# Kernel tuning notes

Measured on AMD Instinct MI355X. Metric: run time of the kernel, lower is better.

Reference implementation:

```python
import jax, jax.numpy as jnp
import numpy as np

EPS_LN = 1e-5  # nn.LayerNorm default eps
EPS_AD = 1e-5  # AdaIN calc_mean_std eps


def calc_mean_std(feat):
    # feat: [B, S, D]; instance-norm style stats per channel over the seq axis
    mean = jnp.mean(feat, axis=1, keepdims=True)
    var = jnp.var(feat, axis=1, keepdims=True, ddof=1)  # torch .var() is unbiased
    return mean, jnp.sqrt(var + EPS_AD)


def adain(content, style):
    c_mean, c_std = calc_mean_std(content)
    s_mean, s_std = calc_mean_std(style)
    return (content - c_mean) / c_std * s_std + s_mean


def layernorm(x, g, b):
    mu = jnp.mean(x, axis=-1, keepdims=True)
    var = jnp.mean(jnp.square(x - mu), axis=-1, keepdims=True)
    return (x - mu) * jax.lax.rsqrt(var + EPS_LN) * g + b


def silu(x):
    return x * jax.nn.sigmoid(x)


def setup_inputs() -> dict:
    B, S, D = 64, 256, 1024
    key = jax.random.key(0)
    ks = jax.random.split(key, 8)
    sc = lambda n: 1.0 / np.sqrt(n)
    return {
        "x": jax.random.normal(ks[0], (B, S, 2 * D), jnp.float32),
        "embed": jax.random.normal(ks[1], (B, S, D), jnp.float32),
        "style_code": jax.random.normal(ks[2], (B, S, D), jnp.float32),
        # conct: Linear(2*dim, dim)
        "Wc": jax.random.normal(ks[3], (D, 2 * D), jnp.float32) * sc(2 * D),
        "bc": jnp.zeros((D,), jnp.float32),
        # emb_fc: Linear(dim, dim)
        "We": jax.random.normal(ks[4], (D, D), jnp.float32) * sc(D),
        "be": jnp.zeros((D,), jnp.float32),
        # fc0: Conv1d(seq0, seq1, 1) -> [seq1, seq0] matrix over the seq axis
        "W0": jax.random.normal(ks[5], (S, S), jnp.float32) * sc(S),
        "b0": jnp.zeros((S,), jnp.float32),
        # fc1: Linear(dim, dim)
        "W1": jax.random.normal(ks[6], (D, D), jnp.float32) * sc(D),
        "b1": jnp.zeros((D,), jnp.float32),
        # LayerNorm affine params
        "g0": jnp.ones((D,), jnp.float32),
        "beta0": jnp.zeros((D,), jnp.float32),
        "g1": jnp.ones((D,), jnp.float32),
        "beta1": jnp.zeros((D,), jnp.float32),
    }


def reference(x, embed, style_code, Wc, bc, We, be, W0, b0, W1, b1, g0, beta0, g1, beta1):
    # conct (first=True): [B,S,2D] -> [B,S,D]
    adain_input = jnp.einsum('bse,de->bsd', x, Wc) + bc
    tmp = adain(adain_input, style_code)  # alpha = 1.0 so tmp replaces adain_input
    x = tmp + (jnp.einsum('bsd,ed->bse', silu(embed), We) + be)
    # block 0: LN -> 1x1 Conv1d over seq axis -> SiLU -> residual
    x_ = layernorm(x, g0, beta0)
    x_ = jnp.einsum('ts,bsd->btd', W0, x_) + b0[:, None]
    x = x + silu(x_)
    # block 1: LN -> Linear over dim axis -> SiLU -> residual
    x_ = layernorm(x, g1, beta1)
    x_ = jnp.einsum('bsd,ed->bse', x_, W1) + b1
    x = x + silu(x_)
    return (x, embed, style_code)
```

## Files before the change

### kernel.cpp

```cpp
#include <hip/hip_runtime.h>
#include <cstddef>
#include <cstdint>

#define BB 64
#define SS 256
#define DD 1024
#define MM (BB * SS)

typedef unsigned short u16;
typedef unsigned int u32;
typedef short bf16x8 __attribute__((ext_vector_type(8)));
typedef float f32x4 __attribute__((ext_vector_type(4)));

__device__ __forceinline__ float silu_f(float v) {
    return v * (1.0f / (1.0f + __expf(-v)));
}

__device__ __forceinline__ int swz4(int r) {
    return ((r >> 2) & 3) ^ (r & 3);
}

__device__ __forceinline__ void splitf(float f, u16& h, u16& l) {
    const u32 b = __float_as_uint(f);
    const u32 hb = b & 0xFFFF0000u;
    const float lf = f - __uint_as_float(hb);
    h = (u16)(hb >> 16);
    l = (u16)(__float_as_uint(lf) >> 16);
}

__device__ __forceinline__ void gll16(const void* g, void* l) {
    __builtin_amdgcn_global_load_lds(
        (const __attribute__((address_space(1))) u32*)g,
        (__attribute__((address_space(3))) u32*)l, 16, 0, 0);
}

__device__ __forceinline__ void cvt16(const float* av, uint4& h0, uint4& h1,
                                      uint4& l0, uint4& l1) {
    u16 hh[16], hl[16];
#pragma unroll
    for (int m = 0; m < 16; ++m) splitf(av[m], hh[m], hl[m]);
    u32 ph[8], pl[8];
#pragma unroll
    for (int m = 0; m < 8; ++m) {
        ph[m] = (u32)hh[2 * m] | ((u32)hh[2 * m + 1] << 16);
        pl[m] = (u32)hl[2 * m] | ((u32)hl[2 * m + 1] << 16);
    }
    h0 = make_uint4(ph[0], ph[1], ph[2], ph[3]);
    h1 = make_uint4(ph[4], ph[5], ph[6], ph[7]);
    l0 = make_uint4(pl[0], pl[1], pl[2], pl[3]);
    l1 = make_uint4(pl[4], pl[5], pl[6], pl[7]);
}

__global__ __launch_bounds__(256)
void split_w(const float* __restrict__ src, u16* __restrict__ dh,
             u16* __restrict__ dl, int k8shift)
{
    const int idx = blockIdx.x * 256 + threadIdx.x;
    const int n = idx >> k8shift;
    const int c = idx & ((1 << k8shift) - 1);
    const int srcc = (c & ~3) | ((c & 3) ^ swz4(n & 15));
    const float* sp = src + ((size_t)n << (k8shift + 3)) + srcc * 8;
    const float4 v0 = *(const float4*)sp;
    const float4 v1 = *(const float4*)(sp + 4);
    const float av[8] = {v0.x, v0.y, v0.z, v0.w, v1.x, v1.y, v1.z, v1.w};
    u16 hh[8], hl[8];
#pragma unroll
    for (int m = 0; m < 8; ++m) splitf(av[m], hh[m], hl[m]);
    u32 ph[4], pl[4];
#pragma unroll
    for (int m = 0; m < 4; ++m) {
        ph[m] = (u32)hh[2 * m] | ((u32)hh[2 * m + 1] << 16);
        pl[m] = (u32)hl[2 * m] | ((u32)hl[2 * m + 1] << 16);
    }
    *(uint4*)&dh[(size_t)idx * 8] = make_uint4(ph[0], ph[1], ph[2], ph[3]);
    *(uint4*)&dl[(size_t)idx * 8] = make_uint4(pl[0], pl[1], pl[2], pl[3]);
}

template<int AM, int BM, int EPI>
__global__ __launch_bounds__(256, (AM == 0 && BM == 0) ? 4 : 3)
void gemm_bf3(const float* __restrict__ A32,
              const u16* __restrict__ Ahg, const u16* __restrict__ Alg,
              const float* __restrict__ B32,
              const u16* __restrict__ Bhg, const u16* __restrict__ Blg,
              const float* __restrict__ bias,
              const float* __restrict__ t0, const float* __restrict__ scl,
              const float* __restrict__ shf,
              const float* __restrict__ resid, float* __restrict__ C,
              int M, int N, int K, long long bsB, long long bsC)
{
    __shared__ u16 lds[16384];

    const int z = blockIdx.z;
    const int nbx = gridDim.x;
    const int nwg = nbx * gridDim.y;
    int lin = blockIdx.y * nbx + blockIdx.x;
    if ((nwg & 7) == 0) {
        const int cpx = nwg >> 3;
        lin = (lin & 7) * cpx + (lin >> 3);
    }
    const int bx = lin % nbx;
    const int by = lin / nbx;
    const int row0 = by * 128, col0 = bx * 128;

    const int tid = threadIdx.x;
    const int lane = tid & 63, wid = tid >> 6;
    const int wr = wid >> 1, wc = wid & 1;
    const int fr = lane & 15, fh = lane >> 4;
    const int fsw = (fh ^ swz4(fr)) * 8;

    const int srow = tid >> 1;
    const int sko = (tid & 1) << 4;
    const int ssw = swz4(srow & 15);
    const int sw0 = srow * 32 + (((sko >> 3) + 0) ^ ssw) * 8;
    const int sw1 = srow * 32 + (((sko >> 3) + 1) ^ ssw) * 8;

    const float* Ag32 = nullptr;
    const float* Bg32 = nullptr;
    if constexpr (AM != 0) Ag32 = A32 + (size_t)(row0 + srow) * K + sko;
    if constexpr (BM != 0) Bg32 = B32 + (size_t)(col0 + srow) * K + sko;

    const u16* gPre = nullptr; int ldsPre = 0;
    const u16* gB = nullptr; int ldsB = 0, sib0 = 0;

    if constexpr (AM == 0) {
        if constexpr (BM == 0) {
            const u16* gs; int base, lb;
            if (wid == 0)      { gs = Ahg; base = row0; lb = 0; }
            else if (wid == 1) { gs = Alg; base = row0; lb = 4096; }
            else if (wid == 2) { gs = Bhg + (size_t)z * (size_t)bsB; base = col0; lb = 8192; }
            else               { gs = Blg + (size_t)z * (size_t)bsB; base = col0; lb = 12288; }
            gPre = gs + (size_t)(base + (lane >> 2)) * K + (lane & 3) * 8;
            ldsPre = lb;
        } else {
            const u16* gs = (wid & 1) ? Alg : Ahg;
            gPre = gs + (size_t)(row0 + (lane >> 2)) * K + (lane & 3) * 8;
            ldsPre = (wid & 1) ? 4096 : 0;
        }
    } else {
        gB = ((wid < 2) ? Bhg : Blg) + (size_t)z * (size_t)bsB
             + (size_t)(col0 + (wid & 1) * 64 + (lane >> 2)) * K + (lane & 3) * 8;
        ldsB = (wid < 2) ? 8192 : 12288;
        sib0 = (wid & 1) * 4;
    }

    f32x4 acc[4][4];
#pragma unroll
    for (int i = 0; i < 4; ++i)
#pragma unroll
        for (int j = 0; j < 4; ++j) acc[i][j] = (f32x4){0.f, 0.f, 0.f, 0.f};

    for (int k0 = 0; k0 < K; k0 += 32) {
        float av[16], bv[16];
        if constexpr (AM != 0) {
            const float4 a0 = *(const float4*)(Ag32 + k0);
            const float4 a1 = *(const float4*)(Ag32 + k0 + 4);
            const float4 a2 = *(const float4*)(Ag32 + k0 + 8);
            const float4 a3 = *(const float4*)(Ag32 + k0 + 12);
            av[0]=a0.x; av[1]=a0.y; av[2]=a0.z; av[3]=a0.w;
            av[4]=a1.x; av[5]=a1.y; av[6]=a1.z; av[7]=a1.w;
            av[8]=a2.x; av[9]=a2.y; av[10]=a2.z; av[11]=a2.w;
            av[12]=a3.x; av[13]=a3.y; av[14]=a3.z; av[15]=a3.w;
            if constexpr (AM == 2) {
#pragma unroll
                for (int m = 0; m < 16; ++m) av[m] = silu_f(av[m]);
            }
        }
        if constexpr (BM != 0) {
            const float4 b0 = *(const float4*)(Bg32 + k0);
            const float4 b1 = *(const float4*)(Bg32 + k0 + 4);
            const float4 b2 = *(const float4*)(Bg32 + k0 + 8);
            const float4 b3 = *(const float4*)(Bg32 + k0 + 12);
            bv[0]=b0.x; bv[1]=b0.y; bv[2]=b0.z; bv[3]=b0.w;
            bv[4]=b1.x; bv[5]=b1.y; bv[6]=b1.z; bv[7]=b1.w;
            bv[8]=b2.x; bv[9]=b2.y; bv[10]=b2.z; bv[11]=b2.w;
            bv[12]=b3.x; bv[13]=b3.y; bv[14]=b3.z; bv[15]=b3.w;
        }

        __syncthreads();

        if constexpr (AM == 0) {
            if constexpr (BM == 0) {
#pragma unroll
                for (int q = 0; q < 8; ++q)
                    gll16(gPre + (size_t)q * 16 * K + k0, &lds[ldsPre + q * 512]);
            } else {
                if (wid < 2) {
#pragma unroll
                    for (int q = 0; q < 8; ++q)
                        gll16(gPre + (size_t)q * 16 * K + k0, &lds[ldsPre + q * 512]);
                }
            }
        } else {
#pragma unroll
            for (int q = 0; q < 4; ++q)
                gll16(gB + (size_t)q * 16 * K + k0, &lds[ldsB + (sib0 + q) * 512]);
        }

        if constexpr (AM != 0) {
            uint4 h0, h1, l0, l1;
            cvt16(av, h0, h1, l0, l1);
            *(uint4*)&lds[sw0] = h0;
            *(uint4*)&lds[sw1] = h1;
            *(uint4*)&lds[4096 + sw0] = l0;
            *(uint4*)&lds[4096 + sw1] = l1;
        }
        if constexpr (BM != 0) {
            uint4 h0, h1, l0, l1;
            cvt16(bv, h0, h1, l0, l1);
            *(uint4*)&lds[8192 + sw0] = h0;
            *(uint4*)&lds[8192 + sw1] = h1;
            *(uint4*)&lds[12288 + sw0] = l0;
            *(uint4*)&lds[12288 + sw1] = l1;
        }
        __syncthreads();

        bf16x8 fah[4], fal[4];
#pragma unroll
        for (int i = 0; i < 4; ++i) {
            const int ao = (wr * 64 + i * 16 + fr) * 32 + fsw;
            fah[i] = *(const bf16x8*)&lds[ao];
            fal[i] = *(const bf16x8*)&lds[4096 + ao];
        }
#pragma unroll
        for (int j = 0; j < 4; ++j) {
            const int bo = (wc * 64 + j * 16 + fr) * 32 + fsw;
            const bf16x8 fbh = *(const bf16x8*)&lds[8192 + bo];
            const bf16x8 fbl = *(const bf16x8*)&lds[12288 + bo];
#pragma unroll
            for (int i = 0; i < 4; ++i) {
                acc[i][j] = __builtin_amdgcn_mfma_f32_16x16x32_bf16(fah[i], fbh, acc[i][j], 0, 0, 0);
                acc[i][j] = __builtin_amdgcn_mfma_f32_16x16x32_bf16(fal[i], fbh, acc[i][j], 0, 0, 0);
                acc[i][j] = __builtin_amdgcn_mfma_f32_16x16x32_bf16(fah[i], fbl, acc[i][j], 0, 0, 0);
            }
        }
    }

    const size_t cz = (size_t)z * (size_t)bsC;
#pragma unroll
    for (int i = 0; i < 4; ++i) {
        const int rbase = row0 + wr * 64 + i * 16 + fh * 4;
#pragma unroll
        for (int j = 0; j < 4; ++j) {
            const int c = col0 + wc * 64 + j * 16 + fr;
            float bcol = 0.f, sc = 0.f, sh = 0.f;
            if constexpr (EPI != 3) bcol = bias[c];
            if constexpr (EPI == 1) {
                const int b = rbase >> 8;
                sc = scl[b * DD + c];
                sh = shf[b * DD + c];
            }
#pragma unroll
            for (int r = 0; r < 4; ++r) {
                const int rr = rbase + r;
                const size_t idx = cz + (size_t)rr * N + c;
                const float t = acc[i][j][r] + ((EPI == 3) ? bias[rr] : bcol);
                if constexpr (EPI == 0) C[idx] = t;
                else if constexpr (EPI == 1) C[idx] = fmaf(t0[idx], sc, sh) + t;
                else C[idx] = resid[idx] + silu_f(t);
            }
        }
    }
}

__global__ __launch_bounds__(256)
void adain_stats(const float* __restrict__ t0, const float* __restrict__ style,
                 float* __restrict__ scl, float* __restrict__ shf)
{
    const int idx = blockIdx.x * 256 + threadIdx.x;
    const int b = idx >> 10;
    const int d = idx & (DD - 1);
    const float* pc = t0    + (size_t)b * SS * DD + d;
    const float* ps = style + (size_t)b * SS * DD + d;
    float sc = 0.f, sc2 = 0.f, ss = 0.f, ss2 = 0.f;
    for (int s = 0; s < SS; ++s) {
        const float c  = pc[(size_t)s * DD];
        const float st = ps[(size_t)s * DD];
        sc += c;  sc2 = fmaf(c, c, sc2);
        ss += st; ss2 = fmaf(st, st, ss2);
    }
    const float mc = sc * (1.0f / SS);
    const float ms = ss * (1.0f / SS);
    float vc = (sc2 - (float)SS * mc * mc) * (1.0f / (SS - 1));
    float vs = (ss2 - (float)SS * ms * ms) * (1.0f / (SS - 1));
    vc = fmaxf(vc, 0.f);
    vs = fmaxf(vs, 0.f);
    const float csd = sqrtf(vc + 1e-5f);
    const float ssd = sqrtf(vs + 1e-5f);
    const float sca = ssd / csd;
    scl[idx] = sca;
    shf[idx] = ms - mc * sca;
}

__global__ __launch_bounds__(256)
void ln_stats(const float* __restrict__ X, float* __restrict__ mu, float* __restrict__ rs)
{
    const int row = blockIdx.x * 4 + (threadIdx.x >> 6);
    const int lane = threadIdx.x & 63;
    const float* xr = X + (size_t)row * DD;
    float sum = 0.f, sq = 0.f;
#pragma unroll
    for (int c = 0; c < 4; ++c) {
        const float4 v = *(const float4*)&xr[c * 256 + lane * 4];
        sum += v.x + v.y + v.z + v.w;
        sq += v.x * v.x + v.y * v.y + v.z * v.z + v.w * v.w;
    }
#pragma unroll
    for (int off = 32; off > 0; off >>= 1) {
        sum += __shfl_down(sum, off, 64);
        sq  += __shfl_down(sq,  off, 64);
    }
    if (lane == 0) {
        const float m = sum * (1.0f / DD);
        float var = sq * (1.0f / DD) - m * m;
        var = fmaxf(var, 0.f);
        mu[row] = m;
        rs[row] = rsqrtf(var + 1e-5f);
    }
}

__global__ __launch_bounds__(256)
void ln_t_split(const float* __restrict__ X, const float* __restrict__ mu,
                const float* __restrict__ rs, const float* __restrict__ g,
                const float* __restrict__ beta,
                u16* __restrict__ yTh, u16* __restrict__ yTl)
{
    __shared__ u16 th[64 * 66];
    __shared__ u16 tl[64 * 66];
    const int b = blockIdx.z;
    const int s0 = blockIdx.y * 64;
    const int d0 = blockIdx.x * 64;
    const int t = threadIdx.x;
    const int sl0 = t >> 4;
    const int dl4 = (t & 15) * 4;
    const float4 gv = *(const float4*)&g[d0 + dl4];
    const float4 bv = *(const float4*)&beta[d0 + dl4];
#pragma unroll
    for (int q = 0; q < 4; ++q) {
        const int s_local = q * 16 + sl0;
        const int row = b * SS + s0 + s_local;
        const float4 v = *(const float4*)&X[(size_t)row * DD + d0 + dl4];
        const float m = mu[row], r = rs[row];
        const float vals[4] = {(v.x - m) * r * gv.x + bv.x, (v.y - m) * r * gv.y + bv.y,
                               (v.z - m) * r * gv.z + bv.z, (v.w - m) * r * gv.w + bv.w};
#pragma unroll
        for (int j = 0; j < 4; ++j) {
            u16 hh, lo;
            splitf(vals[j], hh, lo);
            th[(dl4 + j) * 66 + s_local] = hh;
            tl[(dl4 + j) * 66 + s_local] = lo;
        }
    }
    __syncthreads();
    const int dl = t >> 2;
    const int sc = (t & 3) * 16;
    u32 ah[8], al[8];
#pragma unroll
    for (int jj = 0; jj < 8; ++jj) {
        ah[jj] = *(const u32*)&th[dl * 66 + sc + jj * 2];
        al[jj] = *(const u32*)&tl[dl * 66 + sc + jj * 2];
    }
    const int cc0 = (s0 + sc) >> 3;
    const int swv = swz4(dl & 15);
    const int p0 = (cc0 & ~3) | ((cc0 & 3) ^ swv);
    const int p1 = (cc0 & ~3) | ((((cc0 & 3) + 1)) ^ swv);
    const size_t rb = ((size_t)b * DD + d0 + dl) * SS;
    *(uint4*)&yTh[rb + p0 * 8] = make_uint4(ah[0], ah[1], ah[2], ah[3]);
    *(uint4*)&yTh[rb + p1 * 8] = make_uint4(ah[4], ah[5], ah[6], ah[7]);
    *(uint4*)&yTl[rb + p0 * 8] = make_uint4(al[0], al[1], al[2], al[3]);
    *(uint4*)&yTl[rb + p1 * 8] = make_uint4(al[4], al[5], al[6], al[7]);
}

__global__ __launch_bounds__(256)
void ln_split(const float* __restrict__ X, const float* __restrict__ g,
              const float* __restrict__ beta, u16* __restrict__ zh, u16* __restrict__ zl)
{
    const int row = blockIdx.x * 4 + (threadIdx.x >> 6);
    const int lane = threadIdx.x & 63;
    const float* xr = X + (size_t)row * DD;
    float4 v[4];
    float sum = 0.f, sq = 0.f;
#pragma unroll
    for (int q = 0; q < 4; ++q) {
        v[q] = *(const float4*)&xr[lane * 16 + q * 4];
        sum += v[q].x + v[q].y + v[q].z + v[q].w;
        sq += v[q].x * v[q].x + v[q].y * v[q].y + v[q].z * v[q].z + v[q].w * v[q].w;
    }
#pragma unroll
    for (int off = 32; off > 0; off >>= 1) {
        sum += __shfl_down(sum, off, 64);
        sq  += __shfl_down(sq,  off, 64);
    }
    sum = __shfl(sum, 0, 64);
    sq  = __shfl(sq,  0, 64);
    const float m = sum * (1.0f / DD);
    float var = sq * (1.0f / DD) - m * m;
    var = fmaxf(var, 0.f);
    const float r = rsqrtf(var + 1e-5f);
    float ov[16];
#pragma unroll
    for (int q = 0; q < 4; ++q) {
        const float4 gq = *(const float4*)&g[lane * 16 + q * 4];
        const float4 bq = *(const float4*)&beta[lane * 16 + q * 4];
        ov[q * 4 + 0] = (v[q].x - m) * r * gq.x + bq.x;
        ov[q * 4 + 1] = (v[q].y - m) * r * gq.y + bq.y;
        ov[q * 4 + 2] = (v[q].z - m) * r * gq.z + bq.z;
        ov[q * 4 + 3] = (v[q].w - m) * r * gq.w + bq.w;
    }
    uint4 h0, h1, l0, l1;
    cvt16(ov, h0, h1, l0, l1);
    const int swr = swz4(row & 15);
    const int c0 = lane * 2;
    const int p0 = (c0 & ~3) | ((c0 & 3) ^ swr);
    const int p1 = ((c0 + 1) & ~3) | (((c0 + 1) & 3) ^ swr);
    u16* zr = zh + (size_t)row * DD;
    u16* zr2 = zl + (size_t)row * DD;
    *(uint4*)&zr[p0 * 8]  = h0;
    *(uint4*)&zr[p1 * 8]  = h1;
    *(uint4*)&zr2[p0 * 8] = l0;
    *(uint4*)&zr2[p1 * 8] = l1;
}

__global__ __launch_bounds__(256)
void copy_pass(const float4* __restrict__ emb, const float4* __restrict__ sty,
               float4* __restrict__ out_emb, float4* __restrict__ out_sty)
{
    const int n4 = MM * DD / 4;
    const int stride = gridDim.x * blockDim.x;
    for (int i = blockIdx.x * blockDim.x + threadIdx.x; i < n4; i += stride) {
        out_emb[i] = emb[i];
        out_sty[i] = sty[i];
    }
}

extern "C" void kernel_launch(void* const* d_in, const int* in_sizes, int n_in,
                              void* d_out, int out_size, void* d_ws, size_t ws_size,
                              hipStream_t stream)
{
    const float* x     = (const float*)d_in[0];
    const float* embed = (const float*)d_in[1];
    const float* style = (const float*)d_in[2];
    const float* Wc    = (const float*)d_in[3];
    const float* bc    = (const float*)d_in[4];
    const float* We    = (const float*)d_in[5];
    const float* be    = (const float*)d_in[6];
    const float* W0    = (const float*)d_in[7];
    const float* b0    = (const float*)d_in[8];
    const float* W1    = (const float*)d_in[9];
    const float* b1    = (const float*)d_in[10];
    const float* g0    = (const float*)d_in[11];
    const float* beta0 = (const float*)d_in[12];
    const float* g1    = (const float*)d_in[13];
    const float* beta1 = (const float*)d_in[14];

    float* out     = (float*)d_out;
    float* out_x   = out;
    float* out_emb = out + (size_t)MM * DD;
    float* out_sty = out + (size_t)2 * MM * DD;

    float* buf0 = out_sty;
    float* buf1 = out_emb;

    u16* Wch = (u16*)out_x;
    u16* Wcl = Wch + 2097152;
    u16* Weh = Wcl + 2097152;
    u16* Wel = Weh + 1048576;
    u16* W0h = Wel + 1048576;
    u16* W0l = W0h + 65536;
    float* scl = (float*)(W0l + 65536);
    float* shf = scl + BB * DD;
    float* muv = shf + BB * DD;
    float* rsv = muv + MM;

    u16* yTh = (u16*)buf0;
    u16* yTl = yTh + (size_t)MM * DD;
    u16* zh  = (u16*)buf0;
    u16* zl  = zh + (size_t)MM * DD;

    const dim3 gNT(DD / 128, MM / 128, 1);

    split_w<<<1024, 256, 0, stream>>>(Wc, Wch, Wcl, 8);
    split_w<<<512, 256, 0, stream>>>(We, Weh, Wel, 7);
    split_w<<<32, 256, 0, stream>>>(W0, W0h, W0l, 5);

    gemm_bf3<1, 0, 0><<<gNT, 256, 0, stream>>>(
        x, nullptr, nullptr, nullptr, Wch, Wcl, bc, nullptr, nullptr, nullptr,
        nullptr, buf0, MM, DD, 2 * DD, 0, 0);
    adain_stats<<<BB * DD / 256, 256, 0, stream>>>(buf0, style, scl, shf);
    gemm_bf3<2, 0, 1><<<gNT, 256, 0, stream>>>(
        embed, nullptr, nullptr, nullptr, Weh, Wel, be, buf0, scl, shf,
        nullptr, buf1, MM, DD, DD, 0, 0);
    ln_stats<<<MM / 4, 256, 0, stream>>>(buf1, muv, rsv);
    ln_t_split<<<dim3(16, 4, 64), 256, 0, stream>>>(buf1, muv, rsv, g0, beta0, yTh, yTl);
    gemm_bf3<0, 0, 3><<<dim3(8, 2, 64), 256, 0, stream>>>(
        nullptr, W0h, W0l, nullptr, yTh, yTl, b0, nullptr, nullptr, nullptr,
        buf1, buf1, SS, DD, SS, 262144LL, 262144LL);
    ln_split<<<MM / 4, 256, 0, stream>>>(buf1, g1, beta1, zh, zl);
    gemm_bf3<0, 1, 2><<<gNT, 256, 0, stream>>>(
        nullptr, zh, zl, W1, nullptr, nullptr, b1, nullptr, nullptr, nullptr,
        buf1, out_x, MM, DD, DD, 0, 0);
    copy_pass<<<4096, 256, 0, stream>>>((const float4*)embed, (const float4*)style,
                                        (float4*)out_emb, (float4*)out_sty);
}
```

Before: 988.2 us.

## Prefetch next fp32 K-tile into registers and convert after MFMAs

The fp32 operand loads for the next K step are now issued right after the LDS barrier and converted to bf16 hi/lo after the MFMA block, so global load latency and conversion overlap the matrix math instead of sitting before the barrier. The per-thread staging mapping changes so each wave covers 32 rows with lanes split across k-chunks, and launch bounds are raised to 4 waves per SIMD for all variants. This costs extra live registers for the prefetched and converted values, which together with the tighter launch bound may cause spills.

```diff
diff --git a/kernel.cpp b/kernel.cpp
--- a/kernel.cpp
+++ b/kernel.cpp
@@ -32,6 +32,17 @@
     __builtin_amdgcn_global_load_lds(
         (const __attribute__((address_space(1))) u32*)g,
         (__attribute__((address_space(3))) u32*)l, 16, 0, 0);
+}
+
+__device__ __forceinline__ void load16(const float* p, float* v) {
+    const float4 a0 = *(const float4*)p;
+    const float4 a1 = *(const float4*)(p + 4);
+    const float4 a2 = *(const float4*)(p + 8);
+    const float4 a3 = *(const float4*)(p + 12);
+    v[0]=a0.x; v[1]=a0.y; v[2]=a0.z; v[3]=a0.w;
+    v[4]=a1.x; v[5]=a1.y; v[6]=a1.z; v[7]=a1.w;
+    v[8]=a2.x; v[9]=a2.y; v[10]=a2.z; v[11]=a2.w;
+    v[12]=a3.x; v[13]=a3.y; v[14]=a3.z; v[15]=a3.w;
 }
 
 __device__ __forceinline__ void cvt16(const float* av, uint4& h0, uint4& h1,
@@ -77,7 +88,7 @@
 }
 
 template<int AM, int BM, int EPI>
-__global__ __launch_bounds__(256, (AM == 0 && BM == 0) ? 4 : 3)
+__global__ __launch_bounds__(256, 4)
 void gemm_bf3(const float* __restrict__ A32,
               const u16* __restrict__ Ahg, const u16* __restrict__ Alg,
               const float* __restrict__ B32,
@@ -108,16 +119,16 @@
     const int fr = lane & 15, fh = lane >> 4;
     const int fsw = (fh ^ swz4(fr)) * 8;
 
-    const int srow = tid >> 1;
-    const int sko = (tid & 1) << 4;
+    const int srow = wid * 32 + (lane & 31);
+    const int skc = (lane >> 5) * 2;
     const int ssw = swz4(srow & 15);
-    const int sw0 = srow * 32 + (((sko >> 3) + 0) ^ ssw) * 8;
-    const int sw1 = srow * 32 + (((sko >> 3) + 1) ^ ssw) * 8;
+    const int sw0 = srow * 32 + (((skc + 0) ^ ssw)) * 8;
+    const int sw1 = srow * 32 + (((skc + 1) ^ ssw)) * 8;
 
     const float* Ag32 = nullptr;
     const float* Bg32 = nullptr;
-    if constexpr (AM != 0) Ag32 = A32 + (size_t)(row0 + srow) * K + sko;
-    if constexpr (BM != 0) Bg32 = B32 + (size_t)(col0 + srow) * K + sko;
+    if constexpr (AM != 0) Ag32 = A32 + (size_t)(row0 + srow) * K + skc * 8;
+    if constexpr (BM != 0) Bg32 = B32 + (size_t)(col0 + srow) * K + skc * 8;
 
     const u16* gPre = nullptr; int ldsPre = 0;
     const u16* gB = nullptr; int ldsB = 0, sib0 = 0;
@@ -149,33 +160,22 @@
 #pragma unroll
         for (int j = 0; j < 4; ++j) acc[i][j] = (f32x4){0.f, 0.f, 0.f, 0.f};
 
+    float av[16], bv[16];
+    uint4 cAh0, cAh1, cAl0, cAl1, cBh0, cBh1, cBl0, cBl1;
+    if constexpr (AM != 0) {
+        load16(Ag32, av);
+        if constexpr (AM == 2) {
+#pragma unroll
+            for (int m = 0; m < 16; ++m) av[m] = silu_f(av[m]);
+        }
+        cvt16(av, cAh0, cAh1, cAl0, cAl1);
+    }
+    if constexpr (BM != 0) {
+        load16(Bg32, bv);
+        cvt16(bv, cBh0, cBh1, cBl0, cBl1);
+    }
+
     for (int k0 = 0; k0 < K; k0 += 32) {
-        float av[16], bv[16];
-        if constexpr (AM != 0) {
-            const float4 a0 = *(const float4*)(Ag32 + k0);
-            const float4 a1 = *(const float4*)(Ag32 + k0 + 4);
-            const float4 a2 = *(const float4*)(Ag32 + k0 + 8);
-            const float4 a3 = *(const float4*)(Ag32 + k0 + 12);
-            av[0]=a0.x; av[1]=a0.y; av[2]=a0.z; av[3]=a0.w;
-            av[4]=a1.x; av[5]=a1.y; av[6]=a1.z; av[7]=a1.w;
-            av[8]=a2.x; av[9]=a2.y; av[10]=a2.z; av[11]=a2.w;
-            av[12]=a3.x; av[13]=a3.y; av[14]=a3.z; av[15]=a3.w;
-            if constexpr (AM == 2) {
-#pragma unroll
-                for (int m = 0; m < 16; ++m) av[m] = silu_f(av[m]);
-            }
-        }
-        if constexpr (BM != 0) {
-            const float4 b0 = *(const float4*)(Bg32 + k0);
-            const float4 b1 = *(const float4*)(Bg32 + k0 + 4);
-            const float4 b2 = *(const float4*)(Bg32 + k0 + 8);
-            const float4 b3 = *(const float4*)(Bg32 + k0 + 12);
-            bv[0]=b0.x; bv[1]=b0.y; bv[2]=b0.z; bv[3]=b0.w;
-            bv[4]=b1.x; bv[5]=b1.y; bv[6]=b1.z; bv[7]=b1.w;
-            bv[8]=b2.x; bv[9]=b2.y; bv[10]=b2.z; bv[11]=b2.w;
-            bv[12]=b3.x; bv[13]=b3.y; bv[14]=b3.z; bv[15]=b3.w;
-        }
-
         __syncthreads();
 
         if constexpr (AM == 0) {
@@ -195,24 +195,23 @@
             for (int q = 0; q < 4; ++q)
                 gll16(gB + (size_t)q * 16 * K + k0, &lds[ldsB + (sib0 + q) * 512]);
         }
-
         if constexpr (AM != 0) {
-            uint4 h0, h1, l0, l1;
-            cvt16(av, h0, h1, l0, l1);
-            *(uint4*)&lds[sw0] = h0;
-            *(uint4*)&lds[sw1] = h1;
-            *(uint4*)&lds[4096 + sw0] = l0;
-            *(uint4*)&lds[4096 + sw1] = l1;
+            *(uint4*)&lds[sw0] = cAh0;
+            *(uint4*)&lds[sw1] = cAh1;
+            *(uint4*)&lds[4096 + sw0] = cAl0;
+            *(uint4*)&lds[4096 + sw1] = cAl1;
         }
         if constexpr (BM != 0) {
-            uint4 h0, h1, l0, l1;
-            cvt16(bv, h0, h1, l0, l1);
-            *(uint4*)&lds[8192 + sw0] = h0;
-            *(uint4*)&lds[8192 + sw1] = h1;
-            *(uint4*)&lds[12288 + sw0] = l0;
-            *(uint4*)&lds[12288 + sw1] = l1;
+            *(uint4*)&lds[8192 + sw0] = cBh0;
+            *(uint4*)&lds[8192 + sw1] = cBh1;
+            *(uint4*)&lds[12288 + sw0] = cBl0;
+            *(uint4*)&lds[12288 + sw1] = cBl1;
         }
         __syncthreads();
+
+        const int kn = (k0 + 32 < K) ? k0 + 32 : 0;
+        if constexpr (AM != 0) load16(Ag32 + kn, av);
+        if constexpr (BM != 0) load16(Bg32 + kn, bv);
 
         bf16x8 fah[4], fal[4];
 #pragma unroll
@@ -232,6 +231,17 @@
                 acc[i][j] = __builtin_amdgcn_mfma_f32_16x16x32_bf16(fal[i], fbh, acc[i][j], 0, 0, 0);
                 acc[i][j] = __builtin_amdgcn_mfma_f32_16x16x32_bf16(fah[i], fbl, acc[i][j], 0, 0, 0);
             }
+        }
+
+        if constexpr (AM != 0) {
+            if constexpr (AM == 2) {
+#pragma unroll
+                for (int m = 0; m < 16; ++m) av[m] = silu_f(av[m]);
+            }
+            cvt16(av, cAh0, cAh1, cAl0, cAl1);
+        }
+        if constexpr (BM != 0) {
+            cvt16(bv, cBh0, cBh1, cBl0, cBl1);
         }
     }
 
```

Result: slower. 1.194 ms (+20.8%).
